# Kernel optimization log

Hardware: AMD Instinct MI355X
Metric: run time of the kernel (lower is better)

Reference implementation:

```python
import jax, jax.numpy as jnp
import numpy as np

D_MODEL, N_HEADS, D_K, D_V = 512, 8, 32, 32
LN_EPS = 1e-5


def setup_inputs() -> dict:
    key = jax.random.key(0)
    ks = jax.random.split(key, 12)
    B, L = 4, 2048
    inner = N_HEADS * D_K
    s_in = 1.0 / np.sqrt(D_MODEL)
    s_fc = 1.0 / np.sqrt(inner)
    return {
        "q": jax.random.normal(ks[0], (B, L, D_MODEL), jnp.float32),
        "k": jax.random.normal(ks[1], (B, L, D_MODEL), jnp.float32),
        "v": jax.random.normal(ks[2], (B, L, D_MODEL), jnp.float32),
        "Wq": jax.random.normal(ks[3], (inner, D_MODEL), jnp.float32) * s_in,
        "bq": jax.random.normal(ks[4], (inner,), jnp.float32) * 0.01,
        "Wk": jax.random.normal(ks[5], (inner, D_MODEL), jnp.float32) * s_in,
        "bk": jax.random.normal(ks[6], (inner,), jnp.float32) * 0.01,
        "Wv": jax.random.normal(ks[7], (N_HEADS * D_V, D_MODEL), jnp.float32) * s_in,
        "bv": jax.random.normal(ks[8], (N_HEADS * D_V,), jnp.float32) * 0.01,
        "Wfc": jax.random.normal(ks[9], (D_MODEL, N_HEADS * D_V), jnp.float32) * s_fc,
        "bfc": jax.random.normal(ks[10], (D_MODEL,), jnp.float32) * 0.01,
        "gamma": jnp.ones((D_MODEL,), jnp.float32),
        "beta": jnp.zeros((D_MODEL,), jnp.float32),
    }


def reference(q, k, v, Wq, bq, Wk, bk, Wv, bv, Wfc, bfc, gamma, beta):
    n, l, _ = q.shape
    # Projection output interpreted as (..., d_k, n_heads): head idx is fastest dim
    def split_heads(x, W, b, dh):
        p = x @ W.T + b                     # [n, l, dh*H]
        return p.reshape(n, x.shape[1], dh, N_HEADS).transpose(0, 3, 1, 2)  # [n,H,l,dh]

    qh = split_heads(q, Wq, bq, D_K)
    kh = split_heads(k, Wk, bk, D_K)
    vh = split_heads(v, Wv, bv, D_V)

    scale = 1.0 / jnp.sqrt(jnp.asarray(D_K, q.dtype))
    scores = jnp.einsum('nhqd,nhkd->nhqk', qh, kh) * scale  # [n,H,L,L]
    att = jax.nn.softmax(scores, axis=-1)
    out = jnp.einsum('nhqk,nhkd->nhqd', att, vh)             # [n,H,L,d_v]
    out = out.transpose(0, 2, 1, 3).reshape(n, l, N_HEADS * D_V)

    fc = out @ Wfc.T + bfc
    x = fc + q  # residual
    mean = jnp.mean(x, axis=-1, keepdims=True)
    var = jnp.mean(jnp.square(x - mean), axis=-1, keepdims=True)
    return gamma * (x - mean) / jnp.sqrt(var + LN_EPS) + beta
```

## Files before the change

### kernel.cpp

```cpp
#include <hip/hip_runtime.h>
#include <math.h>

constexpr int Bn = 4, Ln = 2048, DM = 512, NH = 8, DKv = 32, INNER = 256;
constexpr int TTOK = Bn * Ln;
constexpr size_t HEAD_ELEMS = (size_t)Bn * NH * Ln * DKv;


typedef short short8 __attribute__((ext_vector_type(8)));
typedef short short4v __attribute__((ext_vector_type(4)));
typedef float floatx4 __attribute__((ext_vector_type(4)));
typedef float floatx16 __attribute__((ext_vector_type(16)));

constexpr size_t XB_OFF  = 8u * 1024 * 1024;
constexpr size_t WB_OFF  = 12536832;
constexpr size_t WFCB_OFF = WB_OFF + 3 * 131072;

constexpr float C1 = 0.25505654f;

__device__ inline short f2bf(float x) {
  unsigned u = __builtin_bit_cast(unsigned, x);
  unsigned r = (u + 0x7FFFu + ((u >> 16) & 1u)) >> 16;
  return (short)r;
}

__global__ __launch_bounds__(256) void cvtw_kernel(
    const float* __restrict__ Wq, const float* __restrict__ Wk,
    const float* __restrict__ Wv, const float* __restrict__ Wfc,
    short* __restrict__ Wb, short* __restrict__ Wfcb)
{
  const int z = blockIdx.y;
  const float* src = z == 0 ? Wq : (z == 1 ? Wk : (z == 2 ? Wv : Wfc));
  short* dst = z < 3 ? Wb + (size_t)z * 131072 : Wfcb;
  const int idx = (blockIdx.x * 256 + threadIdx.x) * 4;
  float4 x = *(const float4*)&src[idx];
  *(short4v*)&dst[idx] = (short4v){f2bf(x.x), f2bf(x.y), f2bf(x.z), f2bf(x.w)};
}

__global__ __launch_bounds__(256) void proj_kernel(
    const float* __restrict__ q, const float* __restrict__ k, const float* __restrict__ v,
    const short* __restrict__ Wb,
    const float* __restrict__ bq, const float* __restrict__ bk,
    const float* __restrict__ bv,
    short* __restrict__ ws)
{
  const int mat = blockIdx.z;
  const float* X    = mat == 0 ? q  : (mat == 1 ? k  : v);
  const short* W    = Wb + (size_t)mat * 131072;
  const float* bias = mat == 0 ? bq : (mat == 1 ? bk : bv);
  short* outp = ws + (size_t)mat * HEAD_ELEMS;

  const int t0 = blockIdx.x * 64;
  const int c0 = blockIdx.y * 64;
  const int tid = threadIdx.x;
  const int col = tid & 15;
  const int quad = (tid & 63) >> 4;
  const int w = tid >> 6;

  __shared__ short Xs[64 * 136];
  __shared__ short Wsh[64 * 136];

  floatx4 acc[4];
#pragma unroll
  for (int nj = 0; nj < 4; ++nj) acc[nj] = (floatx4){0.f, 0.f, 0.f, 0.f};

  float4 xr[8];
  short8 wr[4];
  auto loadX = [&](int k0) {
#pragma unroll
    for (int j = 0; j < 8; ++j) {
      const int i = tid + j * 256, row = i >> 5, c4 = i & 31;
      xr[j] = *(const float4*)&X[(size_t)(t0 + row) * DM + k0 + c4 * 4];
    }
  };
  auto loadW = [&](int k0) {
#pragma unroll
    for (int j = 0; j < 4; ++j) {
      const int s = tid + j * 256, row = s >> 4, k8 = s & 15;
      wr[j] = *(const short8*)&W[(size_t)(c0 + row) * DM + k0 + k8 * 8];
    }
  };

  loadX(0);
  loadW(0);

  for (int kc = 0; kc < 4; ++kc) {
#pragma unroll
    for (int j = 0; j < 8; ++j) {
      const int i = tid + j * 256, row = i >> 5, c4 = i & 31;
      *(short4v*)&Xs[row * 136 + c4 * 4] =
          (short4v){f2bf(xr[j].x), f2bf(xr[j].y), f2bf(xr[j].z), f2bf(xr[j].w)};
    }
#pragma unroll
    for (int j = 0; j < 4; ++j) {
      const int s = tid + j * 256, row = s >> 4, k8 = s & 15;
      *(short8*)&Wsh[row * 136 + k8 * 8] = wr[j];
    }
    __syncthreads();
    if (kc < 3) {
      loadX((kc + 1) * 128);
      loadW((kc + 1) * 128);
    }
#pragma unroll
    for (int ks = 0; ks < 4; ++ks) {
      short8 a = *(const short8*)&Xs[(w * 16 + col) * 136 + ks * 32 + quad * 8];
#pragma unroll
      for (int nj = 0; nj < 4; ++nj) {
        short8 b = *(const short8*)&Wsh[(nj * 16 + col) * 136 + ks * 32 + quad * 8];
        acc[nj] = __builtin_amdgcn_mfma_f32_16x16x32_bf16(a, b, acc[nj], 0, 0, 0);
      }
    }
    __syncthreads();
  }

#pragma unroll
  for (int nj = 0; nj < 4; ++nj) {
#pragma unroll
    for (int r = 0; r < 4; ++r) {
      const int t = t0 + w * 16 + quad * 4 + r;
      const int n = t >> 11, ll = t & (Ln - 1);
      const int c = c0 + nj * 16 + col;
      const int d = c >> 3, h = c & 7;
      float pv = acc[nj][r] + bias[c];
      if (mat == 0) pv *= C1;
      const short val = f2bf(pv);
      if (mat < 2)
        outp[((size_t)(n * NH + h) * Ln + ll) * DKv + d] = val;
      else
        outp[((size_t)(n * NH + h) * DKv + d) * Ln + ll] = val;
    }
  }
}

__global__ __launch_bounds__(256) void attn_kernel(const short* __restrict__ ws,
                                                   short* __restrict__ O2b)
{
  const int bh = blockIdx.y;
  const int n = bh >> 3, h = bh & 7;
  const int tid = threadIdx.x;
  const int lane = tid & 63;
  const int col = lane & 31;
  const int hf = lane >> 5;
  const int w = tid >> 6;
  const int qi = blockIdx.x * 128 + w * 32 + col;

  const short* Qh = ws;
  const short* Kg = ws + HEAD_ELEMS + (size_t)bh * Ln * DKv;
  const short* Vg = ws + 2 * HEAD_ELEMS + (size_t)bh * DKv * Ln;

  __shared__ short Ks[2][128 * 40];
  __shared__ short Vs[2][32 * 136];

  short8 aq[2];
#pragma unroll
  for (int c = 0; c < 2; ++c)
    aq[c] = *(const short8*)&Qh[(size_t)bh * Ln * DKv + (size_t)qi * DKv + c * 16 + hf * 8];

  short8 ones;
#pragma unroll
  for (int j = 0; j < 8; ++j) ones[j] = (short)0x3F80;

  floatx16 o, ol;
#pragma unroll
  for (int i = 0; i < 16; ++i) { o[i] = 0.f; ol[i] = 0.f; }

  const int kg = tid >> 1, khalf = tid & 1;
  const int krow = (kg & ~12) | ((kg & 4) << 1) | ((kg & 8) >> 1);
  const int kst = krow * 40 + khalf * 16;
  const int vd = tid >> 3, vkb = tid & 7;
  const int vst = vd * 136 + vkb * 16;

  short8 kr0 = *(const short8*)(Kg + kg * 32 + khalf * 16);
  short8 kr1 = *(const short8*)(Kg + kg * 32 + khalf * 16 + 8);
  short8 vr0 = *(const short8*)(Vg + (size_t)vd * Ln + vkb * 16);
  short8 vr1 = *(const short8*)(Vg + (size_t)vd * Ln + vkb * 16 + 8);

  for (int kt = 0; kt < 16; ++kt) {
    short* ksb = Ks[kt & 1];
    short* vsb = Vs[kt & 1];
    *(short8*)&ksb[kst] = kr0;
    *(short8*)&ksb[kst + 8] = kr1;
    *(short8*)&vsb[vst] = vr0;
    *(short8*)&vsb[vst + 8] = vr1;
    __syncthreads();
    if (kt < 15) {
      kr0 = *(const short8*)(Kg + (size_t)(kt + 1) * 4096 + kg * 32 + khalf * 16);
      kr1 = *(const short8*)(Kg + (size_t)(kt + 1) * 4096 + kg * 32 + khalf * 16 + 8);
      vr0 = *(const short8*)(Vg + (size_t)vd * Ln + (kt + 1) * 128 + vkb * 16);
      vr1 = *(const short8*)(Vg + (size_t)vd * Ln + (kt + 1) * 128 + vkb * 16 + 8);
    }

#pragma unroll
    for (int cc = 0; cc < 4; ++cc) {
      floatx16 st;
#pragma unroll
      for (int i = 0; i < 16; ++i) st[i] = 0.f;
      short8 kf0 = *(const short8*)&ksb[(cc * 32 + col) * 40 + hf * 8];
      short8 kf1 = *(const short8*)&ksb[(cc * 32 + col) * 40 + 16 + hf * 8];
      st = __builtin_amdgcn_mfma_f32_32x32x16_bf16(kf0, aq[0], st, 0, 0, 0);
      st = __builtin_amdgcn_mfma_f32_32x32x16_bf16(kf1, aq[1], st, 0, 0, 0);

      float p[16];
#pragma unroll
      for (int i = 0; i < 16; ++i) p[i] = __builtin_amdgcn_exp2f(st[i]);
      short8 pf[2];
#pragma unroll
      for (int half = 0; half < 2; ++half) {
        unsigned u[4];
#pragma unroll
        for (int j = 0; j < 4; ++j)
          u[j] = __builtin_amdgcn_perm(
              __builtin_bit_cast(unsigned, p[half * 8 + 2 * j + 1]),
              __builtin_bit_cast(unsigned, p[half * 8 + 2 * j]), 0x07060302u);
        uint4 uu = make_uint4(u[0], u[1], u[2], u[3]);
        pf[half] = __builtin_bit_cast(short8, uu);
      }

      ol = __builtin_amdgcn_mfma_f32_32x32x16_bf16(ones, pf[0], ol, 0, 0, 0);
      ol = __builtin_amdgcn_mfma_f32_32x32x16_bf16(ones, pf[1], ol, 0, 0, 0);

      short8 va0 = *(const short8*)&vsb[col * 136 + cc * 32 + hf * 8];
      short8 va1 = *(const short8*)&vsb[col * 136 + cc * 32 + 16 + hf * 8];
      o = __builtin_amdgcn_mfma_f32_32x32x16_bf16(va0, pf[0], o, 0, 0, 0);
      o = __builtin_amdgcn_mfma_f32_32x32x16_bf16(va1, pf[1], o, 0, 0, 0);
    }
  }

  const float inv = 1.f / ol[0];
  short* dst = &O2b[((size_t)n * Ln + qi) * INNER + h * DKv];
#pragma unroll
  for (int g4 = 0; g4 < 4; ++g4) {
    short4v pk = (short4v){f2bf(o[g4 * 4 + 0] * inv), f2bf(o[g4 * 4 + 1] * inv),
                           f2bf(o[g4 * 4 + 2] * inv), f2bf(o[g4 * 4 + 3] * inv)};
    *(short4v*)&dst[8 * g4 + 4 * hf] = pk;
  }
}

__global__ __launch_bounds__(256) void fc_kernel(
    const short* __restrict__ O2b, const short* __restrict__ Wfcb,
    const float* __restrict__ bfc, const float* __restrict__ qin,
    short* __restrict__ Xb)
{
  const int t0 = blockIdx.x * 64;
  const int c0 = blockIdx.y * 64;
  const int tid = threadIdx.x;
  const int col = tid & 15;
  const int quad = (tid & 63) >> 4;
  const int w = tid >> 6;

  __shared__ short As[64 * 264];
  __shared__ short Bs[64 * 264];

  for (int i = tid; i < 2048; i += 256) {
    const int row = i >> 5, k8 = i & 31;
    *(short8*)&As[row * 264 + k8 * 8] =
        *(const short8*)&O2b[(size_t)(t0 + row) * INNER + k8 * 8];
    *(short8*)&Bs[row * 264 + k8 * 8] =
        *(const short8*)&Wfcb[(size_t)(c0 + row) * INNER + k8 * 8];
  }
  __syncthreads();

  floatx4 acc[4];
#pragma unroll
  for (int nj = 0; nj < 4; ++nj) acc[nj] = (floatx4){0.f, 0.f, 0.f, 0.f};

#pragma unroll
  for (int ks = 0; ks < 8; ++ks) {
    short8 a = *(const short8*)&As[(w * 16 + col) * 264 + ks * 32 + quad * 8];
#pragma unroll
    for (int nj = 0; nj < 4; ++nj) {
      short8 b = *(const short8*)&Bs[(nj * 16 + col) * 264 + ks * 32 + quad * 8];
      acc[nj] = __builtin_amdgcn_mfma_f32_16x16x32_bf16(a, b, acc[nj], 0, 0, 0);
    }
  }

#pragma unroll
  for (int nj = 0; nj < 4; ++nj) {
#pragma unroll
    for (int r = 0; r < 4; ++r) {
      const int t = t0 + w * 16 + quad * 4 + r;
      const int c = c0 + nj * 16 + col;
      Xb[(size_t)t * DM + c] = f2bf(acc[nj][r] + bfc[c] + qin[(size_t)t * DM + c]);
    }
  }
}

__global__ __launch_bounds__(256) void ln_kernel(
    const short* __restrict__ Xb, const float* __restrict__ gamma,
    const float* __restrict__ beta, float* __restrict__ outp)
{
  const int t = blockIdx.x * 4 + (threadIdx.x >> 6);
  const int lane = threadIdx.x & 63;

  short8 xs = *(const short8*)&Xb[(size_t)t * DM + lane * 8];
  float x[8];
#pragma unroll
  for (int j = 0; j < 8; ++j)
    x[j] = __builtin_bit_cast(float, ((unsigned)(unsigned short)xs[j]) << 16);

  float s1 = 0.f, s2 = 0.f;
#pragma unroll
  for (int j = 0; j < 8; ++j) { s1 += x[j]; s2 += x[j] * x[j]; }
#pragma unroll
  for (int off = 32; off >= 1; off >>= 1) {
    s1 += __shfl_xor(s1, off);
    s2 += __shfl_xor(s2, off);
  }
  const float mean = s1 * (1.f / 512.f);
  const float var = s2 * (1.f / 512.f) - mean * mean;
  const float rstd = rsqrtf(var + 1e-5f);

  float4 g0 = *(const float4*)&gamma[lane * 8];
  float4 g1 = *(const float4*)&gamma[lane * 8 + 4];
  float4 b0 = *(const float4*)&beta[lane * 8];
  float4 b1 = *(const float4*)&beta[lane * 8 + 4];

  float4 y0, y1;
  y0.x = g0.x * (x[0] - mean) * rstd + b0.x;
  y0.y = g0.y * (x[1] - mean) * rstd + b0.y;
  y0.z = g0.z * (x[2] - mean) * rstd + b0.z;
  y0.w = g0.w * (x[3] - mean) * rstd + b0.w;
  y1.x = g1.x * (x[4] - mean) * rstd + b1.x;
  y1.y = g1.y * (x[5] - mean) * rstd + b1.y;
  y1.z = g1.z * (x[6] - mean) * rstd + b1.z;
  y1.w = g1.w * (x[7] - mean) * rstd + b1.w;

  float* drow = &outp[(size_t)t * DM + lane * 8];
  *(float4*)&drow[0] = y0;
  *(float4*)&drow[4] = y1;
}

extern "C" void kernel_launch(void* const* d_in, const int* in_sizes, int n_in,
                              void* d_out, int out_size, void* d_ws, size_t ws_size,
                              hipStream_t stream) {
  const float* q     = (const float*)d_in[0];
  const float* k     = (const float*)d_in[1];
  const float* v     = (const float*)d_in[2];
  const float* Wq    = (const float*)d_in[3];
  const float* bq    = (const float*)d_in[4];
  const float* Wk    = (const float*)d_in[5];
  const float* bk    = (const float*)d_in[6];
  const float* Wv    = (const float*)d_in[7];
  const float* bv    = (const float*)d_in[8];
  const float* Wfc   = (const float*)d_in[9];
  const float* bfc   = (const float*)d_in[10];
  const float* gamma = (const float*)d_in[11];
  const float* beta  = (const float*)d_in[12];

  short* wsS  = (short*)d_ws;
  short* O2b  = wsS + 3 * HEAD_ELEMS;
  short* Xb   = wsS + XB_OFF;
  short* Wb   = wsS + WB_OFF;
  short* Wfcb = wsS + WFCB_OFF;

  cvtw_kernel<<<dim3(128, 4), 256, 0, stream>>>(Wq, Wk, Wv, Wfc, Wb, Wfcb);

  dim3 gp(TTOK / 64, INNER / 64, 3);
  proj_kernel<<<gp, 256, 0, stream>>>(q, k, v, Wb, bq, bk, bv, wsS);

  dim3 gatt(Ln / 128, Bn * NH);
  attn_kernel<<<gatt, 256, 0, stream>>>(wsS, O2b);

  dim3 gfc(TTOK / 64, DM / 64);
  fc_kernel<<<gfc, 256, 0, stream>>>(O2b, Wfcb, bfc, q, Xb);

  ln_kernel<<<TTOK / 4, 256, 0, stream>>>(Xb, gamma, beta, (float*)d_out);
}
```

Before: 185.1 us.

## Fuse FC projection with LayerNorm and coalesce projection head-split stores

The FC GEMM and LayerNorm kernels become one kernel. Each block computes full 512-wide rows for 16 tokens, reduces the row statistics through shuffles and shared memory, and writes the normalized output directly. This removes the bf16 intermediate buffer, one kernel launch, and the extra rounding of the residual sum to bf16. In the projection kernel, the weight rows are permuted so each block owns two whole heads, and the head-split output is staged through shared memory so it can be written with 16-byte coalesced stores instead of scattered 2-byte writes. The trade-off is that FC weights are now read from global memory or L2 by every block without shared staging, and there are fewer, larger FC blocks.

New measurement: 175.2 us. 5.4% less time.

```diff
diff --git a/kernel.cpp b/kernel.cpp
--- a/kernel.cpp
+++ b/kernel.cpp
@@ -11,7 +11,6 @@
 typedef float floatx4 __attribute__((ext_vector_type(4)));
 typedef float floatx16 __attribute__((ext_vector_type(16)));
 
-constexpr size_t XB_OFF  = 8u * 1024 * 1024;
 constexpr size_t WB_OFF  = 12536832;
 constexpr size_t WFCB_OFF = WB_OFF + 3 * 131072;
 
@@ -50,7 +49,7 @@
   short* outp = ws + (size_t)mat * HEAD_ELEMS;
 
   const int t0 = blockIdx.x * 64;
-  const int c0 = blockIdx.y * 64;
+  const int hp = blockIdx.y;
   const int tid = threadIdx.x;
   const int col = tid & 15;
   const int quad = (tid & 63) >> 4;
@@ -76,7 +75,8 @@
 #pragma unroll
     for (int j = 0; j < 4; ++j) {
       const int s = tid + j * 256, row = s >> 4, k8 = s & 15;
-      wr[j] = *(const short8*)&W[(size_t)(c0 + row) * DM + k0 + k8 * 8];
+      const int wrow = ((row & 31) << 3) + 2 * hp + (row >> 5);
+      wr[j] = *(const short8*)&W[(size_t)wrow * DM + k0 + k8 * 8];
     }
   };
 
@@ -112,21 +112,49 @@
     __syncthreads();
   }
 
-#pragma unroll
-  for (int nj = 0; nj < 4; ++nj) {
-#pragma unroll
-    for (int r = 0; r < 4; ++r) {
-      const int t = t0 + w * 16 + quad * 4 + r;
-      const int n = t >> 11, ll = t & (Ln - 1);
-      const int c = c0 + nj * 16 + col;
-      const int d = c >> 3, h = c & 7;
-      float pv = acc[nj][r] + bias[c];
-      if (mat == 0) pv *= C1;
-      const short val = f2bf(pv);
-      if (mat < 2)
-        outp[((size_t)(n * NH + h) * Ln + ll) * DKv + d] = val;
-      else
-        outp[((size_t)(n * NH + h) * DKv + d) * Ln + ll] = val;
+  short* Ct = Xs;
+  const int n = t0 >> 11, llb = t0 & (Ln - 1);
+
+  if (mat < 2) {
+#pragma unroll
+    for (int nj = 0; nj < 4; ++nj) {
+      const int j = nj * 16 + col;
+      const int c = ((j & 31) << 3) + 2 * hp + (j >> 5);
+      const float bi = bias[c];
+#pragma unroll
+      for (int r = 0; r < 4; ++r) {
+        float pv = acc[nj][r] + bi;
+        if (mat == 0) pv *= C1;
+        Ct[(w * 16 + quad * 4 + r) * 72 + j] = f2bf(pv);
+      }
+    }
+    __syncthreads();
+#pragma unroll
+    for (int it = 0; it < 2; ++it) {
+      const int cid = tid + it * 256;
+      const int h_loc = cid >> 8, tok = (cid >> 2) & 63, o = cid & 3;
+      short8 val = *(const short8*)&Ct[tok * 72 + h_loc * 32 + o * 8];
+      const int h = 2 * hp + h_loc;
+      *(short8*)&outp[((size_t)(n * NH + h) * Ln + llb + tok) * DKv + o * 8] = val;
+    }
+  } else {
+#pragma unroll
+    for (int nj = 0; nj < 4; ++nj) {
+      const int j = nj * 16 + col;
+      const int c = ((j & 31) << 3) + 2 * hp + (j >> 5);
+      const float bi = bias[c];
+      short4v pk = (short4v){f2bf(acc[nj][0] + bi), f2bf(acc[nj][1] + bi),
+                             f2bf(acc[nj][2] + bi), f2bf(acc[nj][3] + bi)};
+      *(short4v*)&Ct[j * 72 + w * 16 + quad * 4] = pk;
+    }
+    __syncthreads();
+#pragma unroll
+    for (int it = 0; it < 2; ++it) {
+      const int cid = tid + it * 256;
+      const int h_loc = cid >> 8, d = (cid >> 3) & 31, to = cid & 7;
+      short8 val = *(const short8*)&Ct[(h_loc * 32 + d) * 72 + to * 8];
+      const int h = 2 * hp + h_loc;
+      *(short8*)&outp[((size_t)(n * NH + h) * DKv + d) * Ln + llb + to * 8] = val;
     }
   }
 }
@@ -235,98 +263,101 @@
   }
 }
 
-__global__ __launch_bounds__(256) void fc_kernel(
+__global__ __launch_bounds__(256) void fcln_kernel(
     const short* __restrict__ O2b, const short* __restrict__ Wfcb,
     const float* __restrict__ bfc, const float* __restrict__ qin,
-    short* __restrict__ Xb)
+    const float* __restrict__ gamma, const float* __restrict__ beta,
+    float* __restrict__ outp)
 {
-  const int t0 = blockIdx.x * 64;
-  const int c0 = blockIdx.y * 64;
+  const int t0 = blockIdx.x * 16;
   const int tid = threadIdx.x;
   const int col = tid & 15;
   const int quad = (tid & 63) >> 4;
   const int w = tid >> 6;
 
-  __shared__ short As[64 * 264];
-  __shared__ short Bs[64 * 264];
-
-  for (int i = tid; i < 2048; i += 256) {
-    const int row = i >> 5, k8 = i & 31;
-    *(short8*)&As[row * 264 + k8 * 8] =
-        *(const short8*)&O2b[(size_t)(t0 + row) * INNER + k8 * 8];
-    *(short8*)&Bs[row * 264 + k8 * 8] =
-        *(const short8*)&Wfcb[(size_t)(c0 + row) * INNER + k8 * 8];
+  __shared__ short As[16 * 264];
+  __shared__ float sred[2][16][4];
+
+  {
+    const int row = tid >> 4, k16 = tid & 15;
+    *(short8*)&As[row * 264 + k16 * 16] =
+        *(const short8*)&O2b[(size_t)(t0 + row) * INNER + k16 * 16];
+    *(short8*)&As[row * 264 + k16 * 16 + 8] =
+        *(const short8*)&O2b[(size_t)(t0 + row) * INNER + k16 * 16 + 8];
   }
   __syncthreads();
 
-  floatx4 acc[4];
-#pragma unroll
-  for (int nj = 0; nj < 4; ++nj) acc[nj] = (floatx4){0.f, 0.f, 0.f, 0.f};
+  const short* Wp = Wfcb + (size_t)(w * 128 + col) * INNER + quad * 8;
+
+  floatx4 acc[8];
+#pragma unroll
+  for (int nj = 0; nj < 8; ++nj) acc[nj] = (floatx4){0.f, 0.f, 0.f, 0.f};
 
 #pragma unroll
   for (int ks = 0; ks < 8; ++ks) {
-    short8 a = *(const short8*)&As[(w * 16 + col) * 264 + ks * 32 + quad * 8];
-#pragma unroll
-    for (int nj = 0; nj < 4; ++nj) {
-      short8 b = *(const short8*)&Bs[(nj * 16 + col) * 264 + ks * 32 + quad * 8];
+    short8 a = *(const short8*)&As[col * 264 + ks * 32 + quad * 8];
+#pragma unroll
+    for (int nj = 0; nj < 8; ++nj) {
+      short8 b = *(const short8*)&Wp[(size_t)nj * 16 * INNER + ks * 32];
       acc[nj] = __builtin_amdgcn_mfma_f32_16x16x32_bf16(a, b, acc[nj], 0, 0, 0);
     }
   }
 
-#pragma unroll
-  for (int nj = 0; nj < 4; ++nj) {
+  float s1[4], s2[4];
+#pragma unroll
+  for (int r = 0; r < 4; ++r) { s1[r] = 0.f; s2[r] = 0.f; }
+
+#pragma unroll
+  for (int nj = 0; nj < 8; ++nj) {
+    const int c = w * 128 + nj * 16 + col;
+    const float bi = bfc[c];
 #pragma unroll
     for (int r = 0; r < 4; ++r) {
-      const int t = t0 + w * 16 + quad * 4 + r;
-      const int c = c0 + nj * 16 + col;
-      Xb[(size_t)t * DM + c] = f2bf(acc[nj][r] + bfc[c] + qin[(size_t)t * DM + c]);
-    }
-  }
-}
-
-__global__ __launch_bounds__(256) void ln_kernel(
-    const short* __restrict__ Xb, const float* __restrict__ gamma,
-    const float* __restrict__ beta, float* __restrict__ outp)
-{
-  const int t = blockIdx.x * 4 + (threadIdx.x >> 6);
-  const int lane = threadIdx.x & 63;
-
-  short8 xs = *(const short8*)&Xb[(size_t)t * DM + lane * 8];
-  float x[8];
-#pragma unroll
-  for (int j = 0; j < 8; ++j)
-    x[j] = __builtin_bit_cast(float, ((unsigned)(unsigned short)xs[j]) << 16);
-
-  float s1 = 0.f, s2 = 0.f;
-#pragma unroll
-  for (int j = 0; j < 8; ++j) { s1 += x[j]; s2 += x[j] * x[j]; }
-#pragma unroll
-  for (int off = 32; off >= 1; off >>= 1) {
-    s1 += __shfl_xor(s1, off);
-    s2 += __shfl_xor(s2, off);
-  }
-  const float mean = s1 * (1.f / 512.f);
-  const float var = s2 * (1.f / 512.f) - mean * mean;
-  const float rstd = rsqrtf(var + 1e-5f);
-
-  float4 g0 = *(const float4*)&gamma[lane * 8];
-  float4 g1 = *(const float4*)&gamma[lane * 8 + 4];
-  float4 b0 = *(const float4*)&beta[lane * 8];
-  float4 b1 = *(const float4*)&beta[lane * 8 + 4];
-
-  float4 y0, y1;
-  y0.x = g0.x * (x[0] - mean) * rstd + b0.x;
-  y0.y = g0.y * (x[1] - mean) * rstd + b0.y;
-  y0.z = g0.z * (x[2] - mean) * rstd + b0.z;
-  y0.w = g0.w * (x[3] - mean) * rstd + b0.w;
-  y1.x = g1.x * (x[4] - mean) * rstd + b1.x;
-  y1.y = g1.y * (x[5] - mean) * rstd + b1.y;
-  y1.z = g1.z * (x[6] - mean) * rstd + b1.z;
-  y1.w = g1.w * (x[7] - mean) * rstd + b1.w;
-
-  float* drow = &outp[(size_t)t * DM + lane * 8];
-  *(float4*)&drow[0] = y0;
-  *(float4*)&drow[4] = y1;
+      const int t = t0 + quad * 4 + r;
+      float x = acc[nj][r] + bi + qin[(size_t)t * DM + c];
+      acc[nj][r] = x;
+      s1[r] += x;
+      s2[r] += x * x;
+    }
+  }
+#pragma unroll
+  for (int r = 0; r < 4; ++r) {
+#pragma unroll
+    for (int off = 1; off <= 8; off <<= 1) {
+      s1[r] += __shfl_xor(s1[r], off);
+      s2[r] += __shfl_xor(s2[r], off);
+    }
+  }
+  if (col == 0) {
+#pragma unroll
+    for (int r = 0; r < 4; ++r) {
+      sred[0][quad * 4 + r][w] = s1[r];
+      sred[1][quad * 4 + r][w] = s2[r];
+    }
+  }
+  __syncthreads();
+
+  float mean[4], rstd[4];
+#pragma unroll
+  for (int r = 0; r < 4; ++r) {
+    const int tk = quad * 4 + r;
+    const float S1 = sred[0][tk][0] + sred[0][tk][1] + sred[0][tk][2] + sred[0][tk][3];
+    const float S2 = sred[1][tk][0] + sred[1][tk][1] + sred[1][tk][2] + sred[1][tk][3];
+    mean[r] = S1 * (1.f / 512.f);
+    const float var = S2 * (1.f / 512.f) - mean[r] * mean[r];
+    rstd[r] = rsqrtf(var + 1e-5f);
+  }
+
+#pragma unroll
+  for (int nj = 0; nj < 8; ++nj) {
+    const int c = w * 128 + nj * 16 + col;
+    const float g = gamma[c], bb = beta[c];
+#pragma unroll
+    for (int r = 0; r < 4; ++r) {
+      const int t = t0 + quad * 4 + r;
+      outp[(size_t)t * DM + c] = g * (acc[nj][r] - mean[r]) * rstd[r] + bb;
+    }
+  }
 }
 
 extern "C" void kernel_launch(void* const* d_in, const int* in_sizes, int n_in,
@@ -348,20 +379,17 @@
 
   short* wsS  = (short*)d_ws;
   short* O2b  = wsS + 3 * HEAD_ELEMS;
-  short* Xb   = wsS + XB_OFF;
   short* Wb   = wsS + WB_OFF;
   short* Wfcb = wsS + WFCB_OFF;
 
   cvtw_kernel<<<dim3(128, 4), 256, 0, stream>>>(Wq, Wk, Wv, Wfc, Wb, Wfcb);
 
-  dim3 gp(TTOK / 64, INNER / 64, 3);
+  dim3 gp(TTOK / 64, 4, 3);
   proj_kernel<<<gp, 256, 0, stream>>>(q, k, v, Wb, bq, bk, bv, wsS);
 
   dim3 gatt(Ln / 128, Bn * NH);
   attn_kernel<<<gatt, 256, 0, stream>>>(wsS, O2b);
 
-  dim3 gfc(TTOK / 64, DM / 64);
-  fc_kernel<<<gfc, 256, 0, stream>>>(O2b, Wfcb, bfc, q, Xb);
-
-  ln_kernel<<<TTOK / 4, 256, 0, stream>>>(Xb, gamma, beta, (float*)d_out);
-}
+  fcln_kernel<<<dim3(TTOK / 16), 256, 0, stream>>>(O2b, Wfcb, bfc, q, gamma, beta,
+                                                   (float*)d_out);
+}
```
